# Kernel tuning notes

Hardware: AMD Instinct MI355X
Metric: run time of the kernel (lower is better)

The kernel has to match this reference:

```python
import jax, jax.numpy as jnp
import numpy as np

N_NODES = 50000


def gcn_conv(x, W, b, src, dst):
    # PyG GCNConv: lin (no bias) -> add self-loops -> symmetric deg norm ->
    # scatter-add messages to target nodes -> add bias.
    n = x.shape[0]
    xw = x @ W  # [N, H]
    loops = jnp.arange(n, dtype=src.dtype)
    s = jnp.concatenate([src, loops])
    d = jnp.concatenate([dst, loops])
    deg = jax.ops.segment_sum(jnp.ones(d.shape[0], dtype=x.dtype), d, num_segments=n)
    dinv = deg ** -0.5  # deg >= 1 due to self-loops
    norm = dinv[s] * dinv[d]  # [E+N]
    msg = xw[s] * norm[:, None]  # gather + scale, [E+N, H]
    out = jax.ops.segment_sum(msg, d, num_segments=n)  # scatter-add
    return out + b


def setup_inputs() -> dict:
    key = jax.random.key(0)
    ks = jax.random.split(key, 8)
    in_feats, hidden, out_feats, p = 64, 64, 32, 4
    x = jax.random.normal(ks[0], (N_NODES, in_feats), dtype=jnp.float32)
    edge_index = jax.random.randint(ks[1], (2, 800000), 0, N_NODES, dtype=jnp.int64)
    s1 = (1.0 / in_feats) ** 0.5
    s2 = (1.0 / hidden) ** 0.5
    W1 = jax.random.uniform(ks[2], (in_feats, hidden), jnp.float32, -s1, s1)
    b1 = jnp.zeros((hidden,), jnp.float32)
    W2 = jax.random.uniform(ks[3], (hidden, hidden), jnp.float32, -s2, s2)
    b2 = jnp.zeros((hidden,), jnp.float32)
    Wr = jax.random.uniform(ks[4], (hidden, out_feats * p), jnp.float32, -s2, s2)
    br = jax.random.uniform(ks[5], (out_feats * p,), jnp.float32, -s2, s2)
    return {"x": x, "edge_index": edge_index, "W1": W1, "b1": b1,
            "W2": W2, "b2": b2, "Wr": Wr, "br": br}


def reference(x, edge_index, W1, b1, W2, b2, Wr, br):
    src, dst = edge_index[0], edge_index[1]
    h = jax.nn.relu(gcn_conv(x, W1, b1, src, dst))
    h = jax.nn.relu(gcn_conv(h, W2, b2, src, dst))
    g = jnp.mean(h, axis=0, keepdims=True)  # [1, hidden]
    out = (g @ Wr + br).reshape(32, 4)  # (out_feats, p)
    return out
```

## Files before the change

### kernel.cpp

```cpp
#include <hip/hip_runtime.h>
#include <math.h>


#define CH 4096
#define MAXNB 1024

__device__ __forceinline__ float bf2f(unsigned short u) {
    return __uint_as_float(((unsigned)u) << 16);
}
__device__ __forceinline__ unsigned short f2bf(float x) {
    unsigned b = __float_as_uint(x);
    return (unsigned short)((b + 0x7FFF + ((b >> 16) & 1)) >> 16);
}

__global__ __launch_bounds__(256) void k_bucket_hist(const int* __restrict__ dst,
                                                     int* __restrict__ histmat,
                                                     int E, int NB) {
    __shared__ int ih[MAXNB];
    int t = threadIdx.x;
    for (int k = t; k < NB; k += 256) ih[k] = 0;
    __syncthreads();
    int base = blockIdx.x * CH;
    for (int i = 0; i < CH; i += 256) {
        int e = base + i + t;
        if (e < E) atomicAdd(&ih[dst[e] >> 6], 1);
    }
    __syncthreads();
    for (int k = t; k < NB; k += 256) histmat[(size_t)blockIdx.x * NB + k] = ih[k];
}

__global__ __launch_bounds__(1024) void k_scan(int* __restrict__ histmat,
                                               int* __restrict__ bstart,
                                               int* __restrict__ offsets,
                                               float* __restrict__ g,
                                               int NB, int nch, int E, int n) {
    __shared__ int sc[1024];
    int t = threadIdx.x;
    int run = 0;
    if (t < NB) {
        int b = 0;
        for (; b + 8 <= nch; b += 8) {
            int v[8];
#pragma unroll
            for (int u = 0; u < 8; u++) v[u] = histmat[(size_t)(b + u) * NB + t];
#pragma unroll
            for (int u = 0; u < 8; u++) {
                int x = v[u];
                histmat[(size_t)(b + u) * NB + t] = run;
                run += x;
            }
        }
        for (; b < nch; b++) {
            int x = histmat[(size_t)b * NB + t];
            histmat[(size_t)b * NB + t] = run;
            run += x;
        }
    }
    sc[t] = (t < NB) ? run : 0;
    __syncthreads();
    for (int off = 1; off < 1024; off <<= 1) {
        int x = (t >= off) ? sc[t - off] : 0;
        __syncthreads();
        sc[t] += x;
        __syncthreads();
    }
    if (t < NB) bstart[t] = sc[t] - run;
    if (t == 0) { bstart[NB] = E; offsets[n] = E; }
    if (t < 64) g[t] = 0.f;
}

__global__ __launch_bounds__(256) void k_bucket_scatter(const int* __restrict__ src,
                                                        const int* __restrict__ dst,
                                                        const int* __restrict__ histmat,
                                                        const int* __restrict__ bstart,
                                                        int* __restrict__ staged,
                                                        int E, int NB) {
    __shared__ int cur[MAXNB];
    int t = threadIdx.x;
    for (int k = t; k < NB; k += 256)
        cur[k] = bstart[k] + histmat[(size_t)blockIdx.x * NB + k];
    __syncthreads();
    int base = blockIdx.x * CH;
    for (int i = 0; i < CH; i += 256) {
        int e = base + i + t;
        if (e < E) {
            int d = dst[e];
            int pos = atomicAdd(&cur[d >> 6], 1);
            staged[pos] = (src[e] << 6) | (d & 63);
        }
    }
}

__global__ __launch_bounds__(256) void k_local_sort(const int* __restrict__ staged,
                                                    const int* __restrict__ bstart,
                                                    unsigned short* __restrict__ csr,
                                                    int* __restrict__ offsets,
                                                    float* __restrict__ dinv, int n) {
    __shared__ int cnt[64];
    __shared__ int pos[64];
    __shared__ int cur[64];
    int t = threadIdx.x;
    if (t < 64) cnt[t] = 0;
    __syncthreads();
    int k = blockIdx.x;
    int beg = bstart[k], end = bstart[k + 1];
    for (int e = beg + t; e < end; e += 256) atomicAdd(&cnt[staged[e] & 63], 1);
    __syncthreads();
    if (t == 0) {
        int run = 0;
        for (int i = 0; i < 64; i++) { pos[i] = run; run += cnt[i]; }
    }
    __syncthreads();
    if (t < 64) {
        cur[t] = pos[t];
        int node = k * 64 + t;
        if (node < n) {
            offsets[node] = beg + pos[t];
            dinv[node] = 1.0f / sqrtf((float)(cnt[t] + 1));
        }
    }
    __syncthreads();
    for (int e = beg + t; e < end; e += 256) {
        int pk = staged[e];
        int p = atomicAdd(&cur[pk & 63], 1);
        csr[beg + p] = (unsigned short)(pk >> 6);
    }
}

__global__ __launch_bounds__(256) void k_gemm_scale(const float* __restrict__ X,
                                                    const float* __restrict__ W,
                                                    const float* __restrict__ dinv,
                                                    unsigned short* __restrict__ Y, int n) {
    __shared__ float Ws[64 * 64];
    __shared__ float xs[16][64];
    int t = threadIdx.x, w = t >> 6, f = t & 63;
    const float4* W4 = (const float4*)W;
    float4* Ws4 = (float4*)Ws;
#pragma unroll
    for (int j = 0; j < 4; j++) Ws4[t + 256 * j] = W4[t + 256 * j];
    int r0 = blockIdx.x * 16;
#pragma unroll
    for (int i = 0; i < 4; i++) {
        int r = r0 + w * 4 + i;
        xs[w * 4 + i][f] = (r < n) ? X[(size_t)r * 64 + f] : 0.f;
    }
    __syncthreads();
    float acc[4] = {0.f, 0.f, 0.f, 0.f};
#pragma unroll 8
    for (int k = 0; k < 64; k++) {
        float wv = Ws[k * 64 + f];
#pragma unroll
        for (int i = 0; i < 4; i++) acc[i] += xs[w * 4 + i][k] * wv;
    }
#pragma unroll
    for (int i = 0; i < 4; i++) {
        int r = r0 + w * 4 + i;
        if (r < n) Y[(size_t)r * 64 + f] = f2bf(dinv[r] * acc[i]);
    }
}

__global__ __launch_bounds__(256) void k_agg_fuse(const unsigned short* __restrict__ Y,
                                                  const float* __restrict__ dinv,
                                                  const float* __restrict__ bias,
                                                  const int* __restrict__ offsets,
                                                  const unsigned short* __restrict__ csr,
                                                  const float* __restrict__ W2,
                                                  unsigned short* __restrict__ Yout, int n) {
    __shared__ float Ws[64 * 64];
    __shared__ float hs[4][64];
    const ushort4* Y4 = (const ushort4*)Y;
    int t = threadIdx.x, w = t >> 6, l = t & 63;
    int q = l >> 4, c = l & 15;
    {
        const float4* W4 = (const float4*)W2;
        float4* Ws4 = (float4*)Ws;
#pragma unroll
        for (int j = 0; j < 4; j++) Ws4[t + 256 * j] = W4[t + 256 * j];
    }
    int node = blockIdx.x * 4 + w;
    bool valid = node < n;
    float4 hval = make_float4(0.f, 0.f, 0.f, 0.f);
    float dv = 0.f;
    if (valid) {
        float4 acc = make_float4(0.f, 0.f, 0.f, 0.f);
        if (q == 0) {
            ushort4 u = Y4[(size_t)node * 16 + c];
            acc = make_float4(bf2f(u.x), bf2f(u.y), bf2f(u.z), bf2f(u.w));
        }
        int beg = offsets[node], end = offsets[node + 1];
        for (int j = beg + q; j < end; j += 16) {
#pragma unroll
            for (int u = 0; u < 4; u++) {
                int jj = j + 4 * u;
                if (jj < end) {
                    int s = csr[jj];
                    ushort4 v = Y4[(size_t)s * 16 + c];
                    acc.x += bf2f(v.x); acc.y += bf2f(v.y);
                    acc.z += bf2f(v.z); acc.w += bf2f(v.w);
                }
            }
        }
#pragma unroll
        for (int m = 16; m <= 32; m <<= 1) {
            acc.x += __shfl_xor(acc.x, m);
            acc.y += __shfl_xor(acc.y, m);
            acc.z += __shfl_xor(acc.z, m);
            acc.w += __shfl_xor(acc.w, m);
        }
        dv = dinv[node];
        float4 b4 = ((const float4*)bias)[c];
        hval.x = fmaxf(dv * acc.x + b4.x, 0.f);
        hval.y = fmaxf(dv * acc.y + b4.y, 0.f);
        hval.z = fmaxf(dv * acc.z + b4.z, 0.f);
        hval.w = fmaxf(dv * acc.w + b4.w, 0.f);
    }
    if (q == 0) ((float4*)hs[w])[c] = hval;
    __syncthreads();
    if (valid) {
        float acc2 = 0.f;
#pragma unroll
        for (int m = 0; m < 16; m++) {
            float4 h4 = ((const float4*)hs[w])[m];
            acc2 += h4.x * Ws[(4 * m + 0) * 64 + l] + h4.y * Ws[(4 * m + 1) * 64 + l]
                  + h4.z * Ws[(4 * m + 2) * 64 + l] + h4.w * Ws[(4 * m + 3) * 64 + l];
        }
        Yout[(size_t)node * 64 + l] = f2bf(dv * acc2);
    }
}

__global__ __launch_bounds__(256) void k_agg_pool(const unsigned short* __restrict__ Y,
                                                  const float* __restrict__ dinv,
                                                  const float* __restrict__ bias,
                                                  const int* __restrict__ offsets,
                                                  const unsigned short* __restrict__ csr,
                                                  float* __restrict__ pbuf, int n) {
    __shared__ float4 sm4[4][16];
    const ushort4* Y4 = (const ushort4*)Y;
    int t = threadIdx.x, w = t >> 6, l = t & 63;
    int q = l >> 4, c = l & 15;
    int node = blockIdx.x * 4 + w;
    bool valid = node < n;
    float4 hval = make_float4(0.f, 0.f, 0.f, 0.f);
    if (valid) {
        float4 acc = make_float4(0.f, 0.f, 0.f, 0.f);
        if (q == 0) {
            ushort4 u = Y4[(size_t)node * 16 + c];
            acc = make_float4(bf2f(u.x), bf2f(u.y), bf2f(u.z), bf2f(u.w));
        }
        int beg = offsets[node], end = offsets[node + 1];
        for (int j = beg + q; j < end; j += 16) {
#pragma unroll
            for (int u = 0; u < 4; u++) {
                int jj = j + 4 * u;
                if (jj < end) {
                    int s = csr[jj];
                    ushort4 v = Y4[(size_t)s * 16 + c];
                    acc.x += bf2f(v.x); acc.y += bf2f(v.y);
                    acc.z += bf2f(v.z); acc.w += bf2f(v.w);
                }
            }
        }
#pragma unroll
        for (int m = 16; m <= 32; m <<= 1) {
            acc.x += __shfl_xor(acc.x, m);
            acc.y += __shfl_xor(acc.y, m);
            acc.z += __shfl_xor(acc.z, m);
            acc.w += __shfl_xor(acc.w, m);
        }
        float dv = dinv[node];
        float4 b4 = ((const float4*)bias)[c];
        hval.x = fmaxf(dv * acc.x + b4.x, 0.f);
        hval.y = fmaxf(dv * acc.y + b4.y, 0.f);
        hval.z = fmaxf(dv * acc.z + b4.z, 0.f);
        hval.w = fmaxf(dv * acc.w + b4.w, 0.f);
    }
    if (q == 0) sm4[w][c] = valid ? hval : make_float4(0.f, 0.f, 0.f, 0.f);
    __syncthreads();
    if (t < 16) {
        float4 a = sm4[0][t], b = sm4[1][t], d = sm4[2][t], e = sm4[3][t];
        float4 s;
        s.x = (a.x + b.x) + (d.x + e.x);
        s.y = (a.y + b.y) + (d.y + e.y);
        s.z = (a.z + b.z) + (d.z + e.z);
        s.w = (a.w + b.w) + (d.w + e.w);
        ((float4*)pbuf)[(size_t)blockIdx.x * 16 + t] = s;
    }
}

__global__ void k_mean_final(const float* __restrict__ pbuf, float* __restrict__ g,
                             int nrows) {
    __shared__ float part[256];
    int t = threadIdx.x, w = t >> 6, f = t & 63;
    float local = 0.f;
    for (int r = blockIdx.x * 4 + w; r < nrows; r += gridDim.x * 4)
        local += pbuf[(size_t)r * 64 + f];
    part[t] = local;
    __syncthreads();
    if (w == 0) {
        float tot = part[f] + part[64 + f] + part[128 + f] + part[192 + f];
        atomicAdd(&g[f], tot);
    }
}

__global__ void k_readout(const float* __restrict__ g, const float* __restrict__ Wr,
                          const float* __restrict__ br, float* __restrict__ out,
                          float invn) {
    __shared__ float gl[64];
    int t = threadIdx.x;
    if (t < 64) gl[t] = g[t] * invn;
    __syncthreads();
    float acc = br[t];
#pragma unroll
    for (int k = 0; k < 64; k++) acc += gl[k] * Wr[k * 128 + t];
    out[t] = acc;
}

extern "C" void kernel_launch(void* const* d_in, const int* in_sizes, int n_in,
                              void* d_out, int out_size, void* d_ws, size_t ws_size,
                              hipStream_t stream) {
    const float* x  = (const float*)d_in[0];
    const int*   ei = (const int*)d_in[1];
    const float* W1 = (const float*)d_in[2];
    const float* b1 = (const float*)d_in[3];
    const float* W2 = (const float*)d_in[4];
    const float* b2 = (const float*)d_in[5];
    const float* Wr = (const float*)d_in[6];
    const float* br = (const float*)d_in[7];
    float* out = (float*)d_out;

    int n = in_sizes[0] / 64;
    int E = in_sizes[1] / 2;
    const int* src = ei;
    const int* dst = ei + E;

    int NB  = (n + 63) / 64;
    int nch = (E + CH - 1) / CH;

    char* p = (char*)d_ws;
    unsigned short* y1 = (unsigned short*)p; p += (size_t)n * 64 * sizeof(unsigned short);
    unsigned short* y2 = (unsigned short*)p; p += (size_t)n * 64 * sizeof(unsigned short);
    float* pbuf = (float*)p;   p += (size_t)((n + 3) / 4) * 64 * sizeof(float);
    float* dinv = (float*)p;   p += (size_t)n * sizeof(float);
    float* g = (float*)p;      p += 64 * sizeof(float);
    int* staged = (int*)p;     p += (size_t)E * sizeof(int);
    int* offsets = (int*)p;    p += (size_t)(n + 1) * sizeof(int);
    int* histmat = (int*)p;    p += (size_t)nch * NB * sizeof(int);
    int* bstart = (int*)p;     p += (size_t)(NB + 1) * sizeof(int);
    unsigned short* csr = (unsigned short*)p; p += (size_t)E * sizeof(unsigned short);

    k_bucket_hist<<<nch, 256, 0, stream>>>(dst, histmat, E, NB);
    k_scan<<<1, 1024, 0, stream>>>(histmat, bstart, offsets, g, NB, nch, E, n);
    k_bucket_scatter<<<nch, 256, 0, stream>>>(src, dst, histmat, bstart, staged, E, NB);
    k_local_sort<<<NB, 256, 0, stream>>>(staged, bstart, csr, offsets, dinv, n);

    int gb = (n + 3) / 4;
    k_gemm_scale<<<(n + 15) / 16, 256, 0, stream>>>(x, W1, dinv, y1, n);
    k_agg_fuse<<<gb, 256, 0, stream>>>(y1, dinv, b1, offsets, csr, W2, y2, n);
    k_agg_pool<<<gb, 256, 0, stream>>>(y2, dinv, b2, offsets, csr, pbuf, n);

    k_mean_final<<<64, 256, 0, stream>>>(pbuf, g, gb);
    k_readout<<<1, 128, 0, stream>>>(g, Wr, br, out, 1.0f / (float)n);
}
```

Before: 230.9 us.

## Aggregate directly from bucketed edges with shared-memory atomics, drop local sort

Removes the per-bucket local sort and the CSR/offsets arrays. Degree counting now happens inside the first GEMM kernel, and each aggregation block processes a 64-node bucket straight from the staged edge list. Messages are accumulated with LDS float atomics into a padded tile, and the next layer's W2 transform uses a permuted feature layout. The mean pooling is folded into the second aggregation with 8-way partial atomics, which eliminates the pbuf and mean kernels. The trade-off is heavy LDS atomic traffic, larger LDS usage and fewer, larger blocks (one per bucket) in exchange for fewer launches and less CSR construction work.

```diff
diff --git a/kernel.cpp b/kernel.cpp
--- a/kernel.cpp
+++ b/kernel.cpp
@@ -31,9 +31,8 @@
 
 __global__ __launch_bounds__(1024) void k_scan(int* __restrict__ histmat,
                                                int* __restrict__ bstart,
-                                               int* __restrict__ offsets,
-                                               float* __restrict__ g,
-                                               int NB, int nch, int E, int n) {
+                                               float* __restrict__ gpart,
+                                               int NB, int nch, int E) {
     __shared__ int sc[1024];
     int t = threadIdx.x;
     int run = 0;
@@ -65,8 +64,8 @@
         __syncthreads();
     }
     if (t < NB) bstart[t] = sc[t] - run;
-    if (t == 0) { bstart[NB] = E; offsets[n] = E; }
-    if (t < 64) g[t] = 0.f;
+    if (t == 0) bstart[NB] = E;
+    if (t < 512) gpart[t] = 0.f;
 }
 
 __global__ __launch_bounds__(256) void k_bucket_scatter(const int* __restrict__ src,
@@ -91,223 +90,235 @@
     }
 }
 
-__global__ __launch_bounds__(256) void k_local_sort(const int* __restrict__ staged,
-                                                    const int* __restrict__ bstart,
-                                                    unsigned short* __restrict__ csr,
-                                                    int* __restrict__ offsets,
-                                                    float* __restrict__ dinv, int n) {
-    __shared__ int cnt[64];
-    __shared__ int pos[64];
-    __shared__ int cur[64];
-    int t = threadIdx.x;
-    if (t < 64) cnt[t] = 0;
-    __syncthreads();
-    int k = blockIdx.x;
-    int beg = bstart[k], end = bstart[k + 1];
-    for (int e = beg + t; e < end; e += 256) atomicAdd(&cnt[staged[e] & 63], 1);
-    __syncthreads();
-    if (t == 0) {
-        int run = 0;
-        for (int i = 0; i < 64; i++) { pos[i] = run; run += cnt[i]; }
-    }
-    __syncthreads();
-    if (t < 64) {
-        cur[t] = pos[t];
-        int node = k * 64 + t;
-        if (node < n) {
-            offsets[node] = beg + pos[t];
-            dinv[node] = 1.0f / sqrtf((float)(cnt[t] + 1));
-        }
-    }
-    __syncthreads();
-    for (int e = beg + t; e < end; e += 256) {
-        int pk = staged[e];
-        int p = atomicAdd(&cur[pk & 63], 1);
-        csr[beg + p] = (unsigned short)(pk >> 6);
-    }
-}
-
-__global__ __launch_bounds__(256) void k_gemm_scale(const float* __restrict__ X,
-                                                    const float* __restrict__ W,
-                                                    const float* __restrict__ dinv,
-                                                    unsigned short* __restrict__ Y, int n) {
+__global__ __launch_bounds__(256) void k_dinv_gemm(const float* __restrict__ X,
+                                                   const float* __restrict__ W1,
+                                                   const int* __restrict__ staged,
+                                                   const int* __restrict__ bstart,
+                                                   float* __restrict__ dinv,
+                                                   unsigned short* __restrict__ Y, int n) {
     __shared__ float Ws[64 * 64];
     __shared__ float xs[16][64];
+    __shared__ int cnt[64];
+    __shared__ float dvs[64];
     int t = threadIdx.x, w = t >> 6, f = t & 63;
-    const float4* W4 = (const float4*)W;
-    float4* Ws4 = (float4*)Ws;
-#pragma unroll
-    for (int j = 0; j < 4; j++) Ws4[t + 256 * j] = W4[t + 256 * j];
-    int r0 = blockIdx.x * 16;
-#pragma unroll
-    for (int i = 0; i < 4; i++) {
-        int r = r0 + w * 4 + i;
-        xs[w * 4 + i][f] = (r < n) ? X[(size_t)r * 64 + f] : 0.f;
-    }
-    __syncthreads();
-    float acc[4] = {0.f, 0.f, 0.f, 0.f};
-#pragma unroll 8
-    for (int k = 0; k < 64; k++) {
-        float wv = Ws[k * 64 + f];
-#pragma unroll
-        for (int i = 0; i < 4; i++) acc[i] += xs[w * 4 + i][k] * wv;
-    }
-#pragma unroll
-    for (int i = 0; i < 4; i++) {
-        int r = r0 + w * 4 + i;
-        if (r < n) Y[(size_t)r * 64 + f] = f2bf(dinv[r] * acc[i]);
-    }
-}
-
-__global__ __launch_bounds__(256) void k_agg_fuse(const unsigned short* __restrict__ Y,
-                                                  const float* __restrict__ dinv,
-                                                  const float* __restrict__ bias,
-                                                  const int* __restrict__ offsets,
-                                                  const unsigned short* __restrict__ csr,
-                                                  const float* __restrict__ W2,
-                                                  unsigned short* __restrict__ Yout, int n) {
-    __shared__ float Ws[64 * 64];
-    __shared__ float hs[4][64];
-    const ushort4* Y4 = (const ushort4*)Y;
+    int kb = blockIdx.x;
+    if (t < 64) cnt[t] = 0;
+    {
+        const float4* W4 = (const float4*)W1;
+        float4* Ws4 = (float4*)Ws;
+#pragma unroll
+        for (int j = 0; j < 4; j++) Ws4[t + 256 * j] = W4[t + 256 * j];
+    }
+    __syncthreads();
+    int beg = bstart[kb], end = bstart[kb + 1];
+    for (int e = beg + t; e < end; e += 256) atomicAdd(&cnt[staged[e] & 63], 1);
+    __syncthreads();
+    if (t < 64) {
+        float dv = 1.0f / sqrtf((float)(cnt[t] + 1));
+        dvs[t] = dv;
+        int node = kb * 64 + t;
+        if (node < n) dinv[node] = dv;
+    }
+    __syncthreads();
+    for (int sub = 0; sub < 4; sub++) {
+        int rb = kb * 64 + sub * 16;
+#pragma unroll
+        for (int i = 0; i < 4; i++) {
+            int r = rb + w * 4 + i;
+            xs[w * 4 + i][f] = (r < n) ? X[(size_t)r * 64 + f] : 0.f;
+        }
+        __syncthreads();
+        float acc0 = 0.f, acc1 = 0.f, acc2 = 0.f, acc3 = 0.f;
+#pragma unroll
+        for (int kq = 0; kq < 16; kq++) {
+            float wv0 = Ws[(4 * kq + 0) * 64 + f];
+            float wv1 = Ws[(4 * kq + 1) * 64 + f];
+            float wv2 = Ws[(4 * kq + 2) * 64 + f];
+            float wv3 = Ws[(4 * kq + 3) * 64 + f];
+            float4 x0 = *(const float4*)&xs[w * 4 + 0][4 * kq];
+            float4 x1 = *(const float4*)&xs[w * 4 + 1][4 * kq];
+            float4 x2 = *(const float4*)&xs[w * 4 + 2][4 * kq];
+            float4 x3 = *(const float4*)&xs[w * 4 + 3][4 * kq];
+            acc0 += x0.x * wv0 + x0.y * wv1 + x0.z * wv2 + x0.w * wv3;
+            acc1 += x1.x * wv0 + x1.y * wv1 + x1.z * wv2 + x1.w * wv3;
+            acc2 += x2.x * wv0 + x2.y * wv1 + x2.z * wv2 + x2.w * wv3;
+            acc3 += x3.x * wv0 + x3.y * wv1 + x3.z * wv2 + x3.w * wv3;
+        }
+        float av[4] = {acc0, acc1, acc2, acc3};
+#pragma unroll
+        for (int i = 0; i < 4; i++) {
+            int r = rb + w * 4 + i;
+            if (r < n) Y[(size_t)r * 64 + f] = f2bf(dvs[sub * 16 + w * 4 + i] * av[i]);
+        }
+        __syncthreads();
+    }
+}
+
+__global__ __launch_bounds__(256) void k_agg1(const unsigned short* __restrict__ Yin,
+                                              const float* __restrict__ dinv,
+                                              const float* __restrict__ b1,
+                                              const int* __restrict__ staged,
+                                              const int* __restrict__ bstart,
+                                              const float* __restrict__ W2,
+                                              unsigned short* __restrict__ Yout, int n) {
+    __shared__ float accL[64 * 68];
+    __shared__ float dvs[64];
     int t = threadIdx.x, w = t >> 6, l = t & 63;
-    int q = l >> 4, c = l & 15;
+    int kb = blockIdx.x;
+    for (int i = t; i < 64 * 68; i += 256) accL[i] = 0.f;
+    if (t < 64) {
+        int node = kb * 64 + t;
+        dvs[t] = (node < n) ? dinv[node] : 0.f;
+    }
+    __syncthreads();
+    int beg = bstart[kb], end = bstart[kb + 1];
+    int c = l & 15;
+    int S = t >> 4;
+    const ushort4* Y4 = (const ushort4*)Yin;
+    int eb = beg + S * 4;
+    int pk[4];
+#pragma unroll
+    for (int u = 0; u < 4; u++) pk[u] = (eb + u < end) ? staged[eb + u] : -1;
+    for (; eb < end;) {
+        int en = eb + 64;
+        int pn[4];
+#pragma unroll
+        for (int u = 0; u < 4; u++) pn[u] = (en + u < end) ? staged[en + u] : -1;
+#pragma unroll
+        for (int u = 0; u < 4; u++) {
+            int p = pk[u];
+            if (p >= 0) {
+                int s = p >> 6, dl = p & 63;
+                ushort4 v = Y4[(size_t)s * 16 + c];
+                float* ap = &accL[dl * 68 + c];
+                atomicAdd(ap + 0,  bf2f(v.x));
+                atomicAdd(ap + 16, bf2f(v.y));
+                atomicAdd(ap + 32, bf2f(v.z));
+                atomicAdd(ap + 48, bf2f(v.w));
+            }
+        }
+#pragma unroll
+        for (int u = 0; u < 4; u++) pk[u] = pn[u];
+        eb = en;
+    }
+    __syncthreads();
     {
-        const float4* W4 = (const float4*)W2;
-        float4* Ws4 = (float4*)Ws;
-#pragma unroll
-        for (int j = 0; j < 4; j++) Ws4[t + 256 * j] = W4[t + 256 * j];
-    }
-    int node = blockIdx.x * 4 + w;
-    bool valid = node < n;
-    float4 hval = make_float4(0.f, 0.f, 0.f, 0.f);
-    float dv = 0.f;
-    if (valid) {
-        float4 acc = make_float4(0.f, 0.f, 0.f, 0.f);
-        if (q == 0) {
-            ushort4 u = Y4[(size_t)node * 16 + c];
-            acc = make_float4(bf2f(u.x), bf2f(u.y), bf2f(u.z), bf2f(u.w));
-        }
-        int beg = offsets[node], end = offsets[node + 1];
-        for (int j = beg + q; j < end; j += 16) {
-#pragma unroll
-            for (int u = 0; u < 4; u++) {
-                int jj = j + 4 * u;
-                if (jj < end) {
-                    int s = csr[jj];
-                    ushort4 v = Y4[(size_t)s * 16 + c];
-                    acc.x += bf2f(v.x); acc.y += bf2f(v.y);
-                    acc.z += bf2f(v.z); acc.w += bf2f(v.w);
-                }
+        int m = l;
+        int fm = ((m & 15) << 2) | (m >> 4);
+        float bb = b1[fm];
+#pragma unroll
+        for (int i = 0; i < 16; i++) {
+            int r = w * 16 + i;
+            int node = kb * 64 + r;
+            float dv = dvs[r];
+            float self = (node < n) ? bf2f(Yin[(size_t)node * 64 + fm]) : 0.f;
+            float hv = fmaxf(dv * (accL[r * 68 + m] + self) + bb, 0.f);
+            accL[r * 68 + m] = dv * hv;
+        }
+    }
+    __syncthreads();
+    float wcol[64];
+#pragma unroll
+    for (int m2 = 0; m2 < 64; m2++) {
+        int fm2 = ((m2 & 15) << 2) | (m2 >> 4);
+        wcol[m2] = W2[fm2 * 64 + l];
+    }
+    for (int i = 0; i < 16; i++) {
+        int r = w * 16 + i;
+        int node = kb * 64 + r;
+        float a2 = 0.f;
+#pragma unroll
+        for (int g = 0; g < 16; g++) {
+            float4 h4 = *(const float4*)&accL[r * 68 + 4 * g];
+            a2 += h4.x * wcol[4 * g + 0] + h4.y * wcol[4 * g + 1]
+                + h4.z * wcol[4 * g + 2] + h4.w * wcol[4 * g + 3];
+        }
+        if (node < n) Yout[(size_t)node * 64 + l] = f2bf(a2);
+    }
+}
+
+__global__ __launch_bounds__(256) void k_agg2(const unsigned short* __restrict__ Yin,
+                                              const float* __restrict__ dinv,
+                                              const float* __restrict__ b2,
+                                              const int* __restrict__ staged,
+                                              const int* __restrict__ bstart,
+                                              float* __restrict__ gpart, int n) {
+    __shared__ float accL[64 * 68];
+    __shared__ float dvs[64];
+    __shared__ float part[4][64];
+    int t = threadIdx.x, w = t >> 6, l = t & 63;
+    int kb = blockIdx.x;
+    for (int i = t; i < 64 * 68; i += 256) accL[i] = 0.f;
+    if (t < 64) {
+        int node = kb * 64 + t;
+        dvs[t] = (node < n) ? dinv[node] : 0.f;
+    }
+    __syncthreads();
+    int beg = bstart[kb], end = bstart[kb + 1];
+    int c = l & 15;
+    int S = t >> 4;
+    const ushort4* Y4 = (const ushort4*)Yin;
+    int eb = beg + S * 4;
+    int pk[4];
+#pragma unroll
+    for (int u = 0; u < 4; u++) pk[u] = (eb + u < end) ? staged[eb + u] : -1;
+    for (; eb < end;) {
+        int en = eb + 64;
+        int pn[4];
+#pragma unroll
+        for (int u = 0; u < 4; u++) pn[u] = (en + u < end) ? staged[en + u] : -1;
+#pragma unroll
+        for (int u = 0; u < 4; u++) {
+            int p = pk[u];
+            if (p >= 0) {
+                int s = p >> 6, dl = p & 63;
+                ushort4 v = Y4[(size_t)s * 16 + c];
+                float* ap = &accL[dl * 68 + c];
+                atomicAdd(ap + 0,  bf2f(v.x));
+                atomicAdd(ap + 16, bf2f(v.y));
+                atomicAdd(ap + 32, bf2f(v.z));
+                atomicAdd(ap + 48, bf2f(v.w));
             }
         }
 #pragma unroll
-        for (int m = 16; m <= 32; m <<= 1) {
-            acc.x += __shfl_xor(acc.x, m);
-            acc.y += __shfl_xor(acc.y, m);
-            acc.z += __shfl_xor(acc.z, m);
-            acc.w += __shfl_xor(acc.w, m);
-        }
-        dv = dinv[node];
-        float4 b4 = ((const float4*)bias)[c];
-        hval.x = fmaxf(dv * acc.x + b4.x, 0.f);
-        hval.y = fmaxf(dv * acc.y + b4.y, 0.f);
-        hval.z = fmaxf(dv * acc.z + b4.z, 0.f);
-        hval.w = fmaxf(dv * acc.w + b4.w, 0.f);
-    }
-    if (q == 0) ((float4*)hs[w])[c] = hval;
-    __syncthreads();
-    if (valid) {
-        float acc2 = 0.f;
-#pragma unroll
-        for (int m = 0; m < 16; m++) {
-            float4 h4 = ((const float4*)hs[w])[m];
-            acc2 += h4.x * Ws[(4 * m + 0) * 64 + l] + h4.y * Ws[(4 * m + 1) * 64 + l]
-                  + h4.z * Ws[(4 * m + 2) * 64 + l] + h4.w * Ws[(4 * m + 3) * 64 + l];
-        }
-        Yout[(size_t)node * 64 + l] = f2bf(dv * acc2);
-    }
-}
-
-__global__ __launch_bounds__(256) void k_agg_pool(const unsigned short* __restrict__ Y,
-                                                  const float* __restrict__ dinv,
-                                                  const float* __restrict__ bias,
-                                                  const int* __restrict__ offsets,
-                                                  const unsigned short* __restrict__ csr,
-                                                  float* __restrict__ pbuf, int n) {
-    __shared__ float4 sm4[4][16];
-    const ushort4* Y4 = (const ushort4*)Y;
-    int t = threadIdx.x, w = t >> 6, l = t & 63;
-    int q = l >> 4, c = l & 15;
-    int node = blockIdx.x * 4 + w;
-    bool valid = node < n;
-    float4 hval = make_float4(0.f, 0.f, 0.f, 0.f);
-    if (valid) {
-        float4 acc = make_float4(0.f, 0.f, 0.f, 0.f);
-        if (q == 0) {
-            ushort4 u = Y4[(size_t)node * 16 + c];
-            acc = make_float4(bf2f(u.x), bf2f(u.y), bf2f(u.z), bf2f(u.w));
-        }
-        int beg = offsets[node], end = offsets[node + 1];
-        for (int j = beg + q; j < end; j += 16) {
-#pragma unroll
-            for (int u = 0; u < 4; u++) {
-                int jj = j + 4 * u;
-                if (jj < end) {
-                    int s = csr[jj];
-                    ushort4 v = Y4[(size_t)s * 16 + c];
-                    acc.x += bf2f(v.x); acc.y += bf2f(v.y);
-                    acc.z += bf2f(v.z); acc.w += bf2f(v.w);
-                }
-            }
-        }
-#pragma unroll
-        for (int m = 16; m <= 32; m <<= 1) {
-            acc.x += __shfl_xor(acc.x, m);
-            acc.y += __shfl_xor(acc.y, m);
-            acc.z += __shfl_xor(acc.z, m);
-            acc.w += __shfl_xor(acc.w, m);
-        }
-        float dv = dinv[node];
-        float4 b4 = ((const float4*)bias)[c];
-        hval.x = fmaxf(dv * acc.x + b4.x, 0.f);
-        hval.y = fmaxf(dv * acc.y + b4.y, 0.f);
-        hval.z = fmaxf(dv * acc.z + b4.z, 0.f);
-        hval.w = fmaxf(dv * acc.w + b4.w, 0.f);
-    }
-    if (q == 0) sm4[w][c] = valid ? hval : make_float4(0.f, 0.f, 0.f, 0.f);
-    __syncthreads();
-    if (t < 16) {
-        float4 a = sm4[0][t], b = sm4[1][t], d = sm4[2][t], e = sm4[3][t];
-        float4 s;
-        s.x = (a.x + b.x) + (d.x + e.x);
-        s.y = (a.y + b.y) + (d.y + e.y);
-        s.z = (a.z + b.z) + (d.z + e.z);
-        s.w = (a.w + b.w) + (d.w + e.w);
-        ((float4*)pbuf)[(size_t)blockIdx.x * 16 + t] = s;
-    }
-}
-
-__global__ void k_mean_final(const float* __restrict__ pbuf, float* __restrict__ g,
-                             int nrows) {
-    __shared__ float part[256];
-    int t = threadIdx.x, w = t >> 6, f = t & 63;
+        for (int u = 0; u < 4; u++) pk[u] = pn[u];
+        eb = en;
+    }
+    __syncthreads();
+    int m = l;
+    int fm = ((m & 15) << 2) | (m >> 4);
+    float bb = b2[fm];
     float local = 0.f;
-    for (int r = blockIdx.x * 4 + w; r < nrows; r += gridDim.x * 4)
-        local += pbuf[(size_t)r * 64 + f];
-    part[t] = local;
-    __syncthreads();
-    if (w == 0) {
-        float tot = part[f] + part[64 + f] + part[128 + f] + part[192 + f];
-        atomicAdd(&g[f], tot);
-    }
-}
-
-__global__ void k_readout(const float* __restrict__ g, const float* __restrict__ Wr,
+#pragma unroll
+    for (int i = 0; i < 16; i++) {
+        int r = w * 16 + i;
+        int node = kb * 64 + r;
+        if (node < n) {
+            float dv = dvs[r];
+            float self = bf2f(Yin[(size_t)node * 64 + fm]);
+            local += fmaxf(dv * (accL[r * 68 + m] + self) + bb, 0.f);
+        }
+    }
+    part[w][m] = local;
+    __syncthreads();
+    if (t < 64) {
+        float tot = part[0][t] + part[1][t] + part[2][t] + part[3][t];
+        int fm2 = ((t & 15) << 2) | (t >> 4);
+        atomicAdd(&gpart[((kb & 7) << 6) + fm2], tot);
+    }
+}
+
+__global__ void k_readout(const float* __restrict__ gpart, const float* __restrict__ Wr,
                           const float* __restrict__ br, float* __restrict__ out,
                           float invn) {
     __shared__ float gl[64];
     int t = threadIdx.x;
-    if (t < 64) gl[t] = g[t] * invn;
+    if (t < 64) {
+        float s = 0.f;
+#pragma unroll
+        for (int j = 0; j < 8; j++) s += gpart[j * 64 + t];
+        gl[t] = s * invn;
+    }
     __syncthreads();
     float acc = br[t];
 #pragma unroll
@@ -339,25 +350,17 @@
     char* p = (char*)d_ws;
     unsigned short* y1 = (unsigned short*)p; p += (size_t)n * 64 * sizeof(unsigned short);
     unsigned short* y2 = (unsigned short*)p; p += (size_t)n * 64 * sizeof(unsigned short);
-    float* pbuf = (float*)p;   p += (size_t)((n + 3) / 4) * 64 * sizeof(float);
     float* dinv = (float*)p;   p += (size_t)n * sizeof(float);
-    float* g = (float*)p;      p += 64 * sizeof(float);
+    float* gpart = (float*)p;  p += 512 * sizeof(float);
     int* staged = (int*)p;     p += (size_t)E * sizeof(int);
-    int* offsets = (int*)p;    p += (size_t)(n + 1) * sizeof(int);
     int* histmat = (int*)p;    p += (size_t)nch * NB * sizeof(int);
     int* bstart = (int*)p;     p += (size_t)(NB + 1) * sizeof(int);
-    unsigned short* csr = (unsigned short*)p; p += (size_t)E * sizeof(unsigned short);
 
     k_bucket_hist<<<nch, 256, 0, stream>>>(dst, histmat, E, NB);
-    k_scan<<<1, 1024, 0, stream>>>(histmat, bstart, offsets, g, NB, nch, E, n);
+    k_scan<<<1, 1024, 0, stream>>>(histmat, bstart, gpart, NB, nch, E);
     k_bucket_scatter<<<nch, 256, 0, stream>>>(src, dst, histmat, bstart, staged, E, NB);
-    k_local_sort<<<NB, 256, 0, stream>>>(staged, bstart, csr, offsets, dinv, n);
-
-    int gb = (n + 3) / 4;
-    k_gemm_scale<<<(n + 15) / 16, 256, 0, stream>>>(x, W1, dinv, y1, n);
-    k_agg_fuse<<<gb, 256, 0, stream>>>(y1, dinv, b1, offsets, csr, W2, y2, n);
-    k_agg_pool<<<gb, 256, 0, stream>>>(y2, dinv, b2, offsets, csr, pbuf, n);
-
-    k_mean_final<<<64, 256, 0, stream>>>(pbuf, g, gb);
-    k_readout<<<1, 128, 0, stream>>>(g, Wr, br, out, 1.0f / (float)n);
-}
+    k_dinv_gemm<<<NB, 256, 0, stream>>>(x, W1, staged, bstart, dinv, y1, n);
+    k_agg1<<<NB, 256, 0, stream>>>(y1, dinv, b1, staged, bstart, W2, y2, n);
+    k_agg2<<<NB, 256, 0, stream>>>(y2, dinv, b2, staged, bstart, gpart, n);
+    k_readout<<<1, 128, 0, stream>>>(gpart, Wr, br, out, 1.0f / (float)n);
+}
```

Result: slower. 872.2 us (+277.8%).

## Fuse mean pooling into aggregation via striped atomics; keep W2 column in registers

Applied to the files above, without the earlier changes.

Removes the per-block partial buffer and the separate mean-reduction kernel. k_agg_pool now atomically adds each block's partial sums into one of 8 striped 64-float slots, and k_readout sums those 8 slots. Separately, k_agg_fuse no longer stages the full 64x64 W2 matrix in shared memory; each thread loads its own 64-element column into registers. This cuts one launch, the pbuf traffic and 16KB of LDS per block, at the cost of about 12.5k blocks doing float atomics on 512 addresses and of higher register pressure, which may lower occupancy.

```diff
diff --git a/kernel.cpp b/kernel.cpp
--- a/kernel.cpp
+++ b/kernel.cpp
@@ -32,7 +32,7 @@
 __global__ __launch_bounds__(1024) void k_scan(int* __restrict__ histmat,
                                                int* __restrict__ bstart,
                                                int* __restrict__ offsets,
-                                               float* __restrict__ g,
+                                               float* __restrict__ gpart,
                                                int NB, int nch, int E, int n) {
     __shared__ int sc[1024];
     int t = threadIdx.x;
@@ -66,7 +66,7 @@
     }
     if (t < NB) bstart[t] = sc[t] - run;
     if (t == 0) { bstart[NB] = E; offsets[n] = E; }
-    if (t < 64) g[t] = 0.f;
+    if (t < 512) gpart[t] = 0.f;
 }
 
 __global__ __launch_bounds__(256) void k_bucket_scatter(const int* __restrict__ src,
@@ -166,17 +166,13 @@
                                                   const unsigned short* __restrict__ csr,
                                                   const float* __restrict__ W2,
                                                   unsigned short* __restrict__ Yout, int n) {
-    __shared__ float Ws[64 * 64];
     __shared__ float hs[4][64];
     const ushort4* Y4 = (const ushort4*)Y;
     int t = threadIdx.x, w = t >> 6, l = t & 63;
     int q = l >> 4, c = l & 15;
-    {
-        const float4* W4 = (const float4*)W2;
-        float4* Ws4 = (float4*)Ws;
-#pragma unroll
-        for (int j = 0; j < 4; j++) Ws4[t + 256 * j] = W4[t + 256 * j];
-    }
+    float wcol[64];
+#pragma unroll
+    for (int m = 0; m < 64; m++) wcol[m] = W2[m * 64 + l];
     int node = blockIdx.x * 4 + w;
     bool valid = node < n;
     float4 hval = make_float4(0.f, 0.f, 0.f, 0.f);
@@ -221,8 +217,8 @@
 #pragma unroll
         for (int m = 0; m < 16; m++) {
             float4 h4 = ((const float4*)hs[w])[m];
-            acc2 += h4.x * Ws[(4 * m + 0) * 64 + l] + h4.y * Ws[(4 * m + 1) * 64 + l]
-                  + h4.z * Ws[(4 * m + 2) * 64 + l] + h4.w * Ws[(4 * m + 3) * 64 + l];
+            acc2 += h4.x * wcol[4 * m + 0] + h4.y * wcol[4 * m + 1]
+                  + h4.z * wcol[4 * m + 2] + h4.w * wcol[4 * m + 3];
         }
         Yout[(size_t)node * 64 + l] = f2bf(dv * acc2);
     }
@@ -233,7 +229,7 @@
                                                   const float* __restrict__ bias,
                                                   const int* __restrict__ offsets,
                                                   const unsigned short* __restrict__ csr,
-                                                  float* __restrict__ pbuf, int n) {
+                                                  float* __restrict__ gpart, int n) {
     __shared__ float4 sm4[4][16];
     const ushort4* Y4 = (const ushort4*)Y;
     int t = threadIdx.x, w = t >> 6, l = t & 63;
@@ -283,31 +279,25 @@
         s.y = (a.y + b.y) + (d.y + e.y);
         s.z = (a.z + b.z) + (d.z + e.z);
         s.w = (a.w + b.w) + (d.w + e.w);
-        ((float4*)pbuf)[(size_t)blockIdx.x * 16 + t] = s;
-    }
-}
-
-__global__ void k_mean_final(const float* __restrict__ pbuf, float* __restrict__ g,
-                             int nrows) {
-    __shared__ float part[256];
-    int t = threadIdx.x, w = t >> 6, f = t & 63;
-    float local = 0.f;
-    for (int r = blockIdx.x * 4 + w; r < nrows; r += gridDim.x * 4)
-        local += pbuf[(size_t)r * 64 + f];
-    part[t] = local;
-    __syncthreads();
-    if (w == 0) {
-        float tot = part[f] + part[64 + f] + part[128 + f] + part[192 + f];
-        atomicAdd(&g[f], tot);
-    }
-}
-
-__global__ void k_readout(const float* __restrict__ g, const float* __restrict__ Wr,
+        float* gp = gpart + ((blockIdx.x & 7) << 6) + 4 * t;
+        atomicAdd(gp + 0, s.x);
+        atomicAdd(gp + 1, s.y);
+        atomicAdd(gp + 2, s.z);
+        atomicAdd(gp + 3, s.w);
+    }
+}
+
+__global__ void k_readout(const float* __restrict__ gpart, const float* __restrict__ Wr,
                           const float* __restrict__ br, float* __restrict__ out,
                           float invn) {
     __shared__ float gl[64];
     int t = threadIdx.x;
-    if (t < 64) gl[t] = g[t] * invn;
+    if (t < 64) {
+        float s = 0.f;
+#pragma unroll
+        for (int j = 0; j < 8; j++) s += gpart[j * 64 + t];
+        gl[t] = s * invn;
+    }
     __syncthreads();
     float acc = br[t];
 #pragma unroll
@@ -339,9 +329,8 @@
     char* p = (char*)d_ws;
     unsigned short* y1 = (unsigned short*)p; p += (size_t)n * 64 * sizeof(unsigned short);
     unsigned short* y2 = (unsigned short*)p; p += (size_t)n * 64 * sizeof(unsigned short);
-    float* pbuf = (float*)p;   p += (size_t)((n + 3) / 4) * 64 * sizeof(float);
     float* dinv = (float*)p;   p += (size_t)n * sizeof(float);
-    float* g = (float*)p;      p += 64 * sizeof(float);
+    float* gpart = (float*)p;  p += 512 * sizeof(float);
     int* staged = (int*)p;     p += (size_t)E * sizeof(int);
     int* offsets = (int*)p;    p += (size_t)(n + 1) * sizeof(int);
     int* histmat = (int*)p;    p += (size_t)nch * NB * sizeof(int);
@@ -349,15 +338,14 @@
     unsigned short* csr = (unsigned short*)p; p += (size_t)E * sizeof(unsigned short);
 
     k_bucket_hist<<<nch, 256, 0, stream>>>(dst, histmat, E, NB);
-    k_scan<<<1, 1024, 0, stream>>>(histmat, bstart, offsets, g, NB, nch, E, n);
+    k_scan<<<1, 1024, 0, stream>>>(histmat, bstart, offsets, gpart, NB, nch, E, n);
     k_bucket_scatter<<<nch, 256, 0, stream>>>(src, dst, histmat, bstart, staged, E, NB);
     k_local_sort<<<NB, 256, 0, stream>>>(staged, bstart, csr, offsets, dinv, n);
 
     int gb = (n + 3) / 4;
     k_gemm_scale<<<(n + 15) / 16, 256, 0, stream>>>(x, W1, dinv, y1, n);
     k_agg_fuse<<<gb, 256, 0, stream>>>(y1, dinv, b1, offsets, csr, W2, y2, n);
-    k_agg_pool<<<gb, 256, 0, stream>>>(y2, dinv, b2, offsets, csr, pbuf, n);
-
-    k_mean_final<<<64, 256, 0, stream>>>(pbuf, g, gb);
-    k_readout<<<1, 128, 0, stream>>>(g, Wr, br, out, 1.0f / (float)n);
-}
+    k_agg_pool<<<gb, 256, 0, stream>>>(y2, dinv, b2, offsets, csr, gpart, n);
+
+    k_readout<<<1, 128, 0, stream>>>(gpart, Wr, br, out, 1.0f / (float)n);
+}
```

New measurement: 357.8 us. 1.55x slower.

## Build CSR with global atomics and pack two nodes per wave in aggregation

Applied to the files above, without the earlier changes.

Replaces the four-kernel bucketed CSR build (block histograms, scan, bucket scatter, per-bucket local sort) with a memset, a global-atomic degree count, a single-block scan that also computes offsets and dinv, and a global-atomic scatter of 32-bit source ids. The aim is to cut kernel count and the staging pass. In exchange it adds contended global atomics and leaves neighbour order within a row non-deterministic, so float summation order can vary between runs. The aggregation kernels now give each node half a wave with two edge groups instead of a full wave with four, fitting the small average degree better. The fused layer-2 matmul now relies on wave-synchronous shared-memory access instead of a block barrier.

```diff
diff --git a/kernel.cpp b/kernel.cpp
--- a/kernel.cpp
+++ b/kernel.cpp
@@ -1,9 +1,6 @@
 #include <hip/hip_runtime.h>
 #include <math.h>
 
-
-#define CH 4096
-#define MAXNB 1024
 
 __device__ __forceinline__ float bf2f(unsigned short u) {
     return __uint_as_float(((unsigned)u) << 16);
@@ -13,50 +10,27 @@
     return (unsigned short)((b + 0x7FFF + ((b >> 16) & 1)) >> 16);
 }
 
-__global__ __launch_bounds__(256) void k_bucket_hist(const int* __restrict__ dst,
-                                                     int* __restrict__ histmat,
-                                                     int E, int NB) {
-    __shared__ int ih[MAXNB];
-    int t = threadIdx.x;
-    for (int k = t; k < NB; k += 256) ih[k] = 0;
-    __syncthreads();
-    int base = blockIdx.x * CH;
-    for (int i = 0; i < CH; i += 256) {
-        int e = base + i + t;
-        if (e < E) atomicAdd(&ih[dst[e] >> 6], 1);
-    }
-    __syncthreads();
-    for (int k = t; k < NB; k += 256) histmat[(size_t)blockIdx.x * NB + k] = ih[k];
-}
-
-__global__ __launch_bounds__(1024) void k_scan(int* __restrict__ histmat,
-                                               int* __restrict__ bstart,
-                                               int* __restrict__ offsets,
-                                               float* __restrict__ g,
-                                               int NB, int nch, int E, int n) {
+__global__ __launch_bounds__(256) void k_deg(const int* __restrict__ dst,
+                                             int* __restrict__ deg, int E) {
+    int i = blockIdx.x * 256 + threadIdx.x;
+    int stride = gridDim.x * 256;
+    for (int e = i; e < E; e += stride) atomicAdd(&deg[dst[e]], 1);
+}
+
+__global__ __launch_bounds__(1024) void k_scan2(const int* __restrict__ deg,
+                                                int* __restrict__ offsets,
+                                                int* __restrict__ cur,
+                                                float* __restrict__ dinv,
+                                                float* __restrict__ g,
+                                                int n, int E) {
     __shared__ int sc[1024];
     int t = threadIdx.x;
-    int run = 0;
-    if (t < NB) {
-        int b = 0;
-        for (; b + 8 <= nch; b += 8) {
-            int v[8];
-#pragma unroll
-            for (int u = 0; u < 8; u++) v[u] = histmat[(size_t)(b + u) * NB + t];
-#pragma unroll
-            for (int u = 0; u < 8; u++) {
-                int x = v[u];
-                histmat[(size_t)(b + u) * NB + t] = run;
-                run += x;
-            }
-        }
-        for (; b < nch; b++) {
-            int x = histmat[(size_t)b * NB + t];
-            histmat[(size_t)b * NB + t] = run;
-            run += x;
-        }
-    }
-    sc[t] = (t < NB) ? run : 0;
+    int C = (n + 1023) / 1024;
+    int base = t * C;
+    int lim = base + C; if (lim > n) lim = n;
+    int sum = 0;
+    for (int i = base; i < lim; i++) sum += deg[i];
+    sc[t] = sum;
     __syncthreads();
     for (int off = 1; off < 1024; off <<= 1) {
         int x = (t >= off) ? sc[t - off] : 0;
@@ -64,66 +38,28 @@
         sc[t] += x;
         __syncthreads();
     }
-    if (t < NB) bstart[t] = sc[t] - run;
-    if (t == 0) { bstart[NB] = E; offsets[n] = E; }
+    int run = sc[t] - sum;
+    for (int i = base; i < lim; i++) {
+        int d = deg[i];
+        offsets[i] = run;
+        cur[i] = run;
+        dinv[i] = 1.0f / sqrtf((float)(d + 1));
+        run += d;
+    }
+    if (t == 0) offsets[n] = E;
     if (t < 64) g[t] = 0.f;
 }
 
-__global__ __launch_bounds__(256) void k_bucket_scatter(const int* __restrict__ src,
-                                                        const int* __restrict__ dst,
-                                                        const int* __restrict__ histmat,
-                                                        const int* __restrict__ bstart,
-                                                        int* __restrict__ staged,
-                                                        int E, int NB) {
-    __shared__ int cur[MAXNB];
-    int t = threadIdx.x;
-    for (int k = t; k < NB; k += 256)
-        cur[k] = bstart[k] + histmat[(size_t)blockIdx.x * NB + k];
-    __syncthreads();
-    int base = blockIdx.x * CH;
-    for (int i = 0; i < CH; i += 256) {
-        int e = base + i + t;
-        if (e < E) {
-            int d = dst[e];
-            int pos = atomicAdd(&cur[d >> 6], 1);
-            staged[pos] = (src[e] << 6) | (d & 63);
-        }
-    }
-}
-
-__global__ __launch_bounds__(256) void k_local_sort(const int* __restrict__ staged,
-                                                    const int* __restrict__ bstart,
-                                                    unsigned short* __restrict__ csr,
-                                                    int* __restrict__ offsets,
-                                                    float* __restrict__ dinv, int n) {
-    __shared__ int cnt[64];
-    __shared__ int pos[64];
-    __shared__ int cur[64];
-    int t = threadIdx.x;
-    if (t < 64) cnt[t] = 0;
-    __syncthreads();
-    int k = blockIdx.x;
-    int beg = bstart[k], end = bstart[k + 1];
-    for (int e = beg + t; e < end; e += 256) atomicAdd(&cnt[staged[e] & 63], 1);
-    __syncthreads();
-    if (t == 0) {
-        int run = 0;
-        for (int i = 0; i < 64; i++) { pos[i] = run; run += cnt[i]; }
-    }
-    __syncthreads();
-    if (t < 64) {
-        cur[t] = pos[t];
-        int node = k * 64 + t;
-        if (node < n) {
-            offsets[node] = beg + pos[t];
-            dinv[node] = 1.0f / sqrtf((float)(cnt[t] + 1));
-        }
-    }
-    __syncthreads();
-    for (int e = beg + t; e < end; e += 256) {
-        int pk = staged[e];
-        int p = atomicAdd(&cur[pk & 63], 1);
-        csr[beg + p] = (unsigned short)(pk >> 6);
+__global__ __launch_bounds__(256) void k_scatter2(const int* __restrict__ src,
+                                                  const int* __restrict__ dst,
+                                                  int* __restrict__ cur,
+                                                  int* __restrict__ csr, int E) {
+    int i = blockIdx.x * 256 + threadIdx.x;
+    int stride = gridDim.x * 256;
+    for (int e = i; e < E; e += stride) {
+        int d = dst[e];
+        int pos = atomicAdd(&cur[d], 1);
+        csr[pos] = src[e];
     }
 }
 
@@ -163,24 +99,24 @@
                                                   const float* __restrict__ dinv,
                                                   const float* __restrict__ bias,
                                                   const int* __restrict__ offsets,
-                                                  const unsigned short* __restrict__ csr,
+                                                  const int* __restrict__ csr,
                                                   const float* __restrict__ W2,
                                                   unsigned short* __restrict__ Yout, int n) {
     __shared__ float Ws[64 * 64];
-    __shared__ float hs[4][64];
+    __shared__ float hs[8][64];
     const ushort4* Y4 = (const ushort4*)Y;
     int t = threadIdx.x, w = t >> 6, l = t & 63;
-    int q = l >> 4, c = l & 15;
+    int h = l >> 5, q = (l >> 4) & 1, c = l & 15;
     {
         const float4* W4 = (const float4*)W2;
         float4* Ws4 = (float4*)Ws;
 #pragma unroll
         for (int j = 0; j < 4; j++) Ws4[t + 256 * j] = W4[t + 256 * j];
     }
-    int node = blockIdx.x * 4 + w;
+    __syncthreads();
+    int node = blockIdx.x * 8 + w * 2 + h;
     bool valid = node < n;
     float4 hval = make_float4(0.f, 0.f, 0.f, 0.f);
-    float dv = 0.f;
     if (valid) {
         float4 acc = make_float4(0.f, 0.f, 0.f, 0.f);
         if (q == 0) {
@@ -188,10 +124,10 @@
             acc = make_float4(bf2f(u.x), bf2f(u.y), bf2f(u.z), bf2f(u.w));
         }
         int beg = offsets[node], end = offsets[node + 1];
-        for (int j = beg + q; j < end; j += 16) {
+        for (int j = beg + q * 4; j < end; j += 8) {
 #pragma unroll
             for (int u = 0; u < 4; u++) {
-                int jj = j + 4 * u;
+                int jj = j + u;
                 if (jj < end) {
                     int s = csr[jj];
                     ushort4 v = Y4[(size_t)s * 16 + c];
@@ -200,45 +136,47 @@
                 }
             }
         }
-#pragma unroll
-        for (int m = 16; m <= 32; m <<= 1) {
-            acc.x += __shfl_xor(acc.x, m);
-            acc.y += __shfl_xor(acc.y, m);
-            acc.z += __shfl_xor(acc.z, m);
-            acc.w += __shfl_xor(acc.w, m);
-        }
-        dv = dinv[node];
+        acc.x += __shfl_xor(acc.x, 16);
+        acc.y += __shfl_xor(acc.y, 16);
+        acc.z += __shfl_xor(acc.z, 16);
+        acc.w += __shfl_xor(acc.w, 16);
+        float dv = dinv[node];
         float4 b4 = ((const float4*)bias)[c];
         hval.x = fmaxf(dv * acc.x + b4.x, 0.f);
         hval.y = fmaxf(dv * acc.y + b4.y, 0.f);
         hval.z = fmaxf(dv * acc.z + b4.z, 0.f);
         hval.w = fmaxf(dv * acc.w + b4.w, 0.f);
     }
-    if (q == 0) ((float4*)hs[w])[c] = hval;
-    __syncthreads();
-    if (valid) {
-        float acc2 = 0.f;
-#pragma unroll
-        for (int m = 0; m < 16; m++) {
-            float4 h4 = ((const float4*)hs[w])[m];
-            acc2 += h4.x * Ws[(4 * m + 0) * 64 + l] + h4.y * Ws[(4 * m + 1) * 64 + l]
-                  + h4.z * Ws[(4 * m + 2) * 64 + l] + h4.w * Ws[(4 * m + 3) * 64 + l];
-        }
-        Yout[(size_t)node * 64 + l] = f2bf(dv * acc2);
-    }
+    if (q == 0) ((float4*)hs[w * 2 + h])[c] = hval;
+    float acc2a = 0.f, acc2b = 0.f;
+#pragma unroll
+    for (int m = 0; m < 16; m++) {
+        float4 ha = ((const float4*)hs[w * 2 + 0])[m];
+        float4 hb = ((const float4*)hs[w * 2 + 1])[m];
+        float wv0 = Ws[(4 * m + 0) * 64 + l];
+        float wv1 = Ws[(4 * m + 1) * 64 + l];
+        float wv2 = Ws[(4 * m + 2) * 64 + l];
+        float wv3 = Ws[(4 * m + 3) * 64 + l];
+        acc2a += ha.x * wv0 + ha.y * wv1 + ha.z * wv2 + ha.w * wv3;
+        acc2b += hb.x * wv0 + hb.y * wv1 + hb.z * wv2 + hb.w * wv3;
+    }
+    int nodeA = blockIdx.x * 8 + w * 2;
+    int nodeB = nodeA + 1;
+    if (nodeA < n) Yout[(size_t)nodeA * 64 + l] = f2bf(dinv[nodeA] * acc2a);
+    if (nodeB < n) Yout[(size_t)nodeB * 64 + l] = f2bf(dinv[nodeB] * acc2b);
 }
 
 __global__ __launch_bounds__(256) void k_agg_pool(const unsigned short* __restrict__ Y,
                                                   const float* __restrict__ dinv,
                                                   const float* __restrict__ bias,
                                                   const int* __restrict__ offsets,
-                                                  const unsigned short* __restrict__ csr,
+                                                  const int* __restrict__ csr,
                                                   float* __restrict__ pbuf, int n) {
-    __shared__ float4 sm4[4][16];
+    __shared__ float4 sm4[8][16];
     const ushort4* Y4 = (const ushort4*)Y;
     int t = threadIdx.x, w = t >> 6, l = t & 63;
-    int q = l >> 4, c = l & 15;
-    int node = blockIdx.x * 4 + w;
+    int h = l >> 5, q = (l >> 4) & 1, c = l & 15;
+    int node = blockIdx.x * 8 + w * 2 + h;
     bool valid = node < n;
     float4 hval = make_float4(0.f, 0.f, 0.f, 0.f);
     if (valid) {
@@ -248,10 +186,10 @@
             acc = make_float4(bf2f(u.x), bf2f(u.y), bf2f(u.z), bf2f(u.w));
         }
         int beg = offsets[node], end = offsets[node + 1];
-        for (int j = beg + q; j < end; j += 16) {
+        for (int j = beg + q * 4; j < end; j += 8) {
 #pragma unroll
             for (int u = 0; u < 4; u++) {
-                int jj = j + 4 * u;
+                int jj = j + u;
                 if (jj < end) {
                     int s = csr[jj];
                     ushort4 v = Y4[(size_t)s * 16 + c];
@@ -260,13 +198,10 @@
                 }
             }
         }
-#pragma unroll
-        for (int m = 16; m <= 32; m <<= 1) {
-            acc.x += __shfl_xor(acc.x, m);
-            acc.y += __shfl_xor(acc.y, m);
-            acc.z += __shfl_xor(acc.z, m);
-            acc.w += __shfl_xor(acc.w, m);
-        }
+        acc.x += __shfl_xor(acc.x, 16);
+        acc.y += __shfl_xor(acc.y, 16);
+        acc.z += __shfl_xor(acc.z, 16);
+        acc.w += __shfl_xor(acc.w, 16);
         float dv = dinv[node];
         float4 b4 = ((const float4*)bias)[c];
         hval.x = fmaxf(dv * acc.x + b4.x, 0.f);
@@ -274,15 +209,15 @@
         hval.z = fmaxf(dv * acc.z + b4.z, 0.f);
         hval.w = fmaxf(dv * acc.w + b4.w, 0.f);
     }
-    if (q == 0) sm4[w][c] = valid ? hval : make_float4(0.f, 0.f, 0.f, 0.f);
+    if (q == 0) sm4[w * 2 + h][c] = hval;
     __syncthreads();
     if (t < 16) {
-        float4 a = sm4[0][t], b = sm4[1][t], d = sm4[2][t], e = sm4[3][t];
-        float4 s;
-        s.x = (a.x + b.x) + (d.x + e.x);
-        s.y = (a.y + b.y) + (d.y + e.y);
-        s.z = (a.z + b.z) + (d.z + e.z);
-        s.w = (a.w + b.w) + (d.w + e.w);
+        float4 s = make_float4(0.f, 0.f, 0.f, 0.f);
+#pragma unroll
+        for (int r = 0; r < 8; r++) {
+            float4 a = sm4[r][t];
+            s.x += a.x; s.y += a.y; s.z += a.z; s.w += a.w;
+        }
         ((float4*)pbuf)[(size_t)blockIdx.x * 16 + t] = s;
     }
 }
@@ -333,27 +268,24 @@
     const int* src = ei;
     const int* dst = ei + E;
 
-    int NB  = (n + 63) / 64;
-    int nch = (E + CH - 1) / CH;
+    int gb = (n + 7) / 8;
 
     char* p = (char*)d_ws;
     unsigned short* y1 = (unsigned short*)p; p += (size_t)n * 64 * sizeof(unsigned short);
     unsigned short* y2 = (unsigned short*)p; p += (size_t)n * 64 * sizeof(unsigned short);
-    float* pbuf = (float*)p;   p += (size_t)((n + 3) / 4) * 64 * sizeof(float);
+    float* pbuf = (float*)p;   p += (size_t)gb * 64 * sizeof(float);
     float* dinv = (float*)p;   p += (size_t)n * sizeof(float);
     float* g = (float*)p;      p += 64 * sizeof(float);
-    int* staged = (int*)p;     p += (size_t)E * sizeof(int);
+    int* deg = (int*)p;        p += (size_t)n * sizeof(int);
+    int* cur = (int*)p;        p += (size_t)n * sizeof(int);
     int* offsets = (int*)p;    p += (size_t)(n + 1) * sizeof(int);
-    int* histmat = (int*)p;    p += (size_t)nch * NB * sizeof(int);
-    int* bstart = (int*)p;     p += (size_t)(NB + 1) * sizeof(int);
-    unsigned short* csr = (unsigned short*)p; p += (size_t)E * sizeof(unsigned short);
-
-    k_bucket_hist<<<nch, 256, 0, stream>>>(dst, histmat, E, NB);
-    k_scan<<<1, 1024, 0, stream>>>(histmat, bstart, offsets, g, NB, nch, E, n);
-    k_bucket_scatter<<<nch, 256, 0, stream>>>(src, dst, histmat, bstart, staged, E, NB);
-    k_local_sort<<<NB, 256, 0, stream>>>(staged, bstart, csr, offsets, dinv, n);
-
-    int gb = (n + 3) / 4;
+    int* csr = (int*)p;        p += (size_t)E * sizeof(int);
+
+    hipMemsetAsync(deg, 0, (size_t)n * sizeof(int), stream);
+    k_deg<<<1024, 256, 0, stream>>>(dst, deg, E);
+    k_scan2<<<1, 1024, 0, stream>>>(deg, offsets, cur, dinv, g, n, E);
+    k_scatter2<<<1024, 256, 0, stream>>>(src, dst, cur, csr, E);
+
     k_gemm_scale<<<(n + 15) / 16, 256, 0, stream>>>(x, W1, dinv, y1, n);
     k_agg_fuse<<<gb, 256, 0, stream>>>(y1, dinv, b1, offsets, csr, W2, y2, n);
     k_agg_pool<<<gb, 256, 0, stream>>>(y2, dinv, b2, offsets, csr, pbuf, n);
```

Measured after the change: 432.7 us. +87.4%, slower.
